# Kernel optimization log

Hardware: AMD Instinct MI355X
Metric: run time of the kernel (lower is better)

Reference implementation:

```python
import jax, jax.numpy as jnp
import numpy as np

N_NODES = 50000
N_EDGES = 800000
IN_DIM, HID_DIM, OUT_DIM = 256, 128, 64


def gcn_conv(x, edge_index, W, b):
    """PyG GCNConv: out = D^{-1/2} (A + I) D^{-1/2} (x @ W) + b."""
    n = x.shape[0]
    loops = jnp.arange(n, dtype=edge_index.dtype)
    src = jnp.concatenate([edge_index[0], loops])  # message source j
    dst = jnp.concatenate([edge_index[1], loops])  # aggregation target i
    ones = jnp.ones(src.shape[0], dtype=x.dtype)
    deg = jax.ops.segment_sum(ones, dst, num_segments=n)  # >= 1 (self-loops)
    dinv = jax.lax.rsqrt(deg)
    norm = dinv[src] * dinv[dst]                    # [E+N]
    h = x @ W                                       # [N, out] GEMM first (PyG order)
    msg = h[src] * norm[:, None]                    # gather + scale
    out = jax.ops.segment_sum(msg, dst, num_segments=n)  # scatter-add
    return out + b


def setup_inputs() -> dict:
    key = jax.random.key(0)
    k1, k2, k3, k4, k5 = jax.random.split(key, 5)
    x = jax.random.normal(k1, (N_NODES, IN_DIM), dtype=jnp.float32)
    edge_index = jax.random.randint(k2, (2, N_EDGES), 0, N_NODES, dtype=jnp.int64)
    # Glorot-ish init for weights, zero bias (PyG defaults)
    W1 = jax.random.normal(k3, (IN_DIM, HID_DIM), dtype=jnp.float32) / np.sqrt(IN_DIM)
    b1 = jnp.zeros((HID_DIM,), dtype=jnp.float32)
    W2 = jax.random.normal(k4, (HID_DIM, OUT_DIM), dtype=jnp.float32) / np.sqrt(HID_DIM)
    b2 = jnp.zeros((OUT_DIM,), dtype=jnp.float32)
    return {"x": x, "edge_index": edge_index, "W1": W1, "b1": b1, "W2": W2, "b2": b2}


def reference(x, edge_index, W1, b1, W2, b2):
    h = jax.nn.relu(gcn_conv(x, edge_index, W1, b1))
    return gcn_conv(h, edge_index, W2, b2)
```

## Files before the change

kernel.cpp:

```cpp
#include <hip/hip_runtime.h>

#define N_NODES 50000
#define N_EDGES 800000
#define IN_DIM 256
#define HID_DIM 128
#define OUT_DIM 64
#define CAP 64

typedef __bf16 bf16x8 __attribute__((ext_vector_type(8)));
typedef float f32x4 __attribute__((ext_vector_type(4)));
typedef unsigned short u16x8 __attribute__((ext_vector_type(8)));
typedef unsigned short ushort_t;
typedef unsigned int uint_t;

__device__ __forceinline__ ushort_t f2bf(float f) {
    uint_t u = __float_as_uint(f);
    return (ushort_t)((u + 0x7fffu + ((u >> 16) & 1u)) >> 16);
}
__device__ __forceinline__ float bf_lo(uint_t u) { return __uint_as_float(u << 16); }
__device__ __forceinline__ float bf_hi(uint_t u) { return __uint_as_float(u & 0xffff0000u); }

__global__ __launch_bounds__(256) void k_init(const float* __restrict__ W1,
                                              ushort_t* __restrict__ w1t,
                                              const float* __restrict__ W2,
                                              ushort_t* __restrict__ w2t) {
    const int bid = blockIdx.x;
    const int t = threadIdx.x;
    if (bid < 128) {
        int id = bid * 256 + t;
        int k = id >> 7, c = id & 127;
        w1t[c * IN_DIM + k] = f2bf(W1[id]);
    } else {
        int id = (bid - 128) * 256 + t;
        int k = id >> 6, c = id & 63;
        w2t[c * HID_DIM + k] = f2bf(W2[id]);
    }
}

__global__ __launch_bounds__(256) void k_bucket(const int* __restrict__ srcs,
                                                const int* __restrict__ dsts,
                                                int* __restrict__ cur,
                                                int* __restrict__ es) {
    int e = blockIdx.x * 256 + threadIdx.x;
    int d = dsts[e];
    int s = srcs[e];
    int p = atomicAdd(&cur[d << 4], 1);
    if (p < CAP) es[d * CAP + p] = s;
}

__global__ __launch_bounds__(256) void k_dinv(const int* __restrict__ cur,
                                              float* __restrict__ dinv,
                                              int* __restrict__ ndeg) {
    int i = blockIdx.x * 256 + threadIdx.x;
    if (i < N_NODES) {
        int deg = cur[i << 4];
        dinv[i] = rsqrtf((float)(deg + 1));
        ndeg[i] = min(deg, CAP);
    }
}

__global__ __launch_bounds__(64) void k_gemm1(const float* __restrict__ x,
                                              const ushort_t* __restrict__ w1t,
                                              ushort_t* __restrict__ hb) {
    const int lane = threadIdx.x;
    const int l15 = lane & 15, quad = lane >> 4;
    const int row = blockIdx.x * 16 + l15;
    f32x4 acc[8];
#pragma unroll
    for (int n = 0; n < 8; ++n) acc[n] = (f32x4){0.f, 0.f, 0.f, 0.f};
    const float* xrow = x + (size_t)row * IN_DIM + quad * 8;
    const ushort_t* wbase = w1t + quad * 8;
#pragma unroll
    for (int t = 0; t < 8; ++t) {
        const float4* xp = (const float4*)(xrow + t * 32);
        float4 f0 = xp[0], f1 = xp[1];
        u16x8 au;
        au[0] = f2bf(f0.x); au[1] = f2bf(f0.y); au[2] = f2bf(f0.z); au[3] = f2bf(f0.w);
        au[4] = f2bf(f1.x); au[5] = f2bf(f1.y); au[6] = f2bf(f1.z); au[7] = f2bf(f1.w);
        bf16x8 a = __builtin_bit_cast(bf16x8, au);
#pragma unroll
        for (int n = 0; n < 8; ++n) {
            bf16x8 b = *(const bf16x8*)(wbase + (n * 16 + l15) * IN_DIM + t * 32);
            acc[n] = __builtin_amdgcn_mfma_f32_16x16x32_bf16(a, b, acc[n], 0, 0, 0);
        }
    }
    ushort_t* hrow = hb + ((size_t)blockIdx.x * 16 + quad * 4) * HID_DIM + l15;
#pragma unroll
    for (int n = 0; n < 8; ++n)
#pragma unroll
        for (int r = 0; r < 4; ++r)
            hrow[(size_t)r * HID_DIM + n * 16] = f2bf(acc[n][r]);
}

__global__ __launch_bounds__(256) void k_agg1(const ushort_t* __restrict__ hb,
                                              const int* __restrict__ ndeg,
                                              const float* __restrict__ dinv,
                                              const int* __restrict__ es,
                                              const float* __restrict__ b,
                                              ushort_t* __restrict__ hrelu) {
    const int i = blockIdx.x * 4 + (threadIdx.x >> 6);
    const int lane = threadIdx.x & 63;
    const float dv = dinv[i];
    const int n = ndeg[i];
    int   sj = 0;
    float nmj = 0.f;
    if (lane < n) {
        sj = es[i * CAP + lane];
        nmj = dinv[sj] * dv;
    }
    uint_t u = *(const uint_t*)(hb + (size_t)i * HID_DIM + 2 * lane);
    float a0 = bf_lo(u) * dv * dv;
    float a1 = bf_hi(u) * dv * dv;
    int j = 0;
    for (; j + 4 <= n; j += 4) {
        int s0 = __shfl(sj, j),     s1 = __shfl(sj, j + 1);
        int s2 = __shfl(sj, j + 2), s3 = __shfl(sj, j + 3);
        float m0 = __shfl(nmj, j),     m1 = __shfl(nmj, j + 1);
        float m2 = __shfl(nmj, j + 2), m3 = __shfl(nmj, j + 3);
        uint_t v0 = *(const uint_t*)(hb + (size_t)s0 * HID_DIM + 2 * lane);
        uint_t v1 = *(const uint_t*)(hb + (size_t)s1 * HID_DIM + 2 * lane);
        uint_t v2 = *(const uint_t*)(hb + (size_t)s2 * HID_DIM + 2 * lane);
        uint_t v3 = *(const uint_t*)(hb + (size_t)s3 * HID_DIM + 2 * lane);
        a0 += bf_lo(v0) * m0 + bf_lo(v1) * m1 + bf_lo(v2) * m2 + bf_lo(v3) * m3;
        a1 += bf_hi(v0) * m0 + bf_hi(v1) * m1 + bf_hi(v2) * m2 + bf_hi(v3) * m3;
    }
    for (; j < n; ++j) {
        int s = __shfl(sj, j);
        float nm = __shfl(nmj, j);
        uint_t v = *(const uint_t*)(hb + (size_t)s * HID_DIM + 2 * lane);
        a0 += bf_lo(v) * nm;
        a1 += bf_hi(v) * nm;
    }
    float v0 = a0 + b[2 * lane];     v0 = v0 > 0.f ? v0 : 0.f;
    float v1 = a1 + b[2 * lane + 1]; v1 = v1 > 0.f ? v1 : 0.f;
    *(uint_t*)(hrelu + (size_t)i * HID_DIM + 2 * lane) = ((uint_t)f2bf(v1) << 16) | f2bf(v0);
}

__global__ __launch_bounds__(64) void k_gemm2(const ushort_t* __restrict__ hrelu,
                                              const ushort_t* __restrict__ w2t,
                                              ushort_t* __restrict__ h2) {
    const int lane = threadIdx.x;
    const int l15 = lane & 15, quad = lane >> 4;
    const int row = blockIdx.x * 16 + l15;
    f32x4 acc[4];
#pragma unroll
    for (int n = 0; n < 4; ++n) acc[n] = (f32x4){0.f, 0.f, 0.f, 0.f};
    const ushort_t* arow = hrelu + (size_t)row * HID_DIM + quad * 8;
    const ushort_t* wbase = w2t + quad * 8;
#pragma unroll
    for (int t = 0; t < 4; ++t) {
        bf16x8 a = *(const bf16x8*)(arow + t * 32);
#pragma unroll
        for (int n = 0; n < 4; ++n) {
            bf16x8 b = *(const bf16x8*)(wbase + (n * 16 + l15) * HID_DIM + t * 32);
            acc[n] = __builtin_amdgcn_mfma_f32_16x16x32_bf16(a, b, acc[n], 0, 0, 0);
        }
    }
    ushort_t* orow = h2 + ((size_t)blockIdx.x * 16 + quad * 4) * OUT_DIM + l15;
#pragma unroll
    for (int n = 0; n < 4; ++n)
#pragma unroll
        for (int r = 0; r < 4; ++r)
            orow[(size_t)r * OUT_DIM + n * 16] = f2bf(acc[n][r]);
}

__global__ __launch_bounds__(256) void k_agg2(const ushort_t* __restrict__ h2,
                                              const int* __restrict__ ndeg,
                                              const float* __restrict__ dinv,
                                              const int* __restrict__ es,
                                              const float* __restrict__ b,
                                              float* __restrict__ out) {
    const int i = blockIdx.x * 4 + (threadIdx.x >> 6);
    const int lane = threadIdx.x & 63;
    const float dv = dinv[i];
    const int n = ndeg[i];
    int   sj = 0;
    float nmj = 0.f;
    if (lane < n) {
        sj = es[i * CAP + lane];
        nmj = dinv[sj] * dv;
    }
    float acc = __uint_as_float(((uint_t)h2[(size_t)i * OUT_DIM + lane]) << 16) * dv * dv;
    int j = 0;
    for (; j + 4 <= n; j += 4) {
        int s0 = __shfl(sj, j),     s1 = __shfl(sj, j + 1);
        int s2 = __shfl(sj, j + 2), s3 = __shfl(sj, j + 3);
        float m0 = __shfl(nmj, j),     m1 = __shfl(nmj, j + 1);
        float m2 = __shfl(nmj, j + 2), m3 = __shfl(nmj, j + 3);
        float v0 = __uint_as_float(((uint_t)h2[(size_t)s0 * OUT_DIM + lane]) << 16);
        float v1 = __uint_as_float(((uint_t)h2[(size_t)s1 * OUT_DIM + lane]) << 16);
        float v2 = __uint_as_float(((uint_t)h2[(size_t)s2 * OUT_DIM + lane]) << 16);
        float v3 = __uint_as_float(((uint_t)h2[(size_t)s3 * OUT_DIM + lane]) << 16);
        acc += v0 * m0 + v1 * m1 + v2 * m2 + v3 * m3;
    }
    for (; j < n; ++j) {
        int s = __shfl(sj, j);
        float nm = __shfl(nmj, j);
        acc += __uint_as_float(((uint_t)h2[(size_t)s * OUT_DIM + lane]) << 16) * nm;
    }
    out[(size_t)i * OUT_DIM + lane] = acc + b[lane];
}

extern "C" void kernel_launch(void* const* d_in, const int* in_sizes, int n_in,
                              void* d_out, int out_size, void* d_ws, size_t ws_size,
                              hipStream_t stream) {
    const float* x   = (const float*)d_in[0];
    const int*   ei  = (const int*)d_in[1];
    const float* W1  = (const float*)d_in[2];
    const float* b1  = (const float*)d_in[3];
    const float* W2  = (const float*)d_in[4];
    const float* b2  = (const float*)d_in[5];
    float* out = (float*)d_out;

    const int* srcs = ei;
    const int* dsts = ei + N_EDGES;

    char* ws = (char*)d_ws;
    size_t o = 0;
    auto alloc = [&](size_t bytes) { void* p = ws + o; o = (o + bytes + 511) & ~size_t(511); return p; };
    int*      cur   = (int*)     alloc((size_t)N_NODES * 16 * 4);
    float*    dinv  = (float*)   alloc(N_NODES * 4);
    int*      ndeg  = (int*)     alloc(N_NODES * 4);
    int*      es    = (int*)     alloc((size_t)N_NODES * CAP * 4);
    ushort_t* w1t   = (ushort_t*)alloc((size_t)IN_DIM * HID_DIM * 2);
    ushort_t* w2t   = (ushort_t*)alloc((size_t)HID_DIM * OUT_DIM * 2);
    ushort_t* hb    = (ushort_t*)alloc((size_t)N_NODES * HID_DIM * 2);
    ushort_t* hrelu = (ushort_t*)alloc((size_t)N_NODES * HID_DIM * 2);
    ushort_t* h2    = (ushort_t*)alloc((size_t)N_NODES * OUT_DIM * 2);

    hipMemsetAsync(cur, 0, (size_t)N_NODES * 16 * 4, stream);
    k_init  <<<160, 256, 0, stream>>>(W1, w1t, W2, w2t);
    k_bucket<<<3125, 256, 0, stream>>>(srcs, dsts, cur, es);
    k_dinv  <<<196, 256, 0, stream>>>(cur, dinv, ndeg);
    k_gemm1 <<<N_NODES / 16, 64, 0, stream>>>(x, w1t, hb);
    k_agg1  <<<N_NODES / 4, 256, 0, stream>>>(hb, ndeg, dinv, es, b1, hrelu);
    k_gemm2 <<<N_NODES / 16, 64, 0, stream>>>(hrelu, w2t, h2);
    k_agg2  <<<N_NODES / 4, 256, 0, stream>>>(h2, ndeg, dinv, es, b2, out);
}
```

Measured before the change: 249.7 us.

## Store edge sources as uint16, fuse dinv into GEMM1, unroll gathers by eight

Edge source indices in the bucket table are stored as 16-bit values instead of 32-bit, halving the bucket write and read traffic. Each bucketing thread now handles two edges. The degree/dinv computation moves into the first GEMM kernel, removing one launch. The aggregation loops gain an 8-wide unrolled gather to keep more loads in flight. The uint16 cast truncates node ids above 65535 only if N_NODES grows; at 50000 nodes it is exact.

```diff
diff --git a/kernel.cpp b/kernel.cpp
--- a/kernel.cpp
+++ b/kernel.cpp
@@ -6,6 +6,7 @@
 #define HID_DIM 128
 #define OUT_DIM 64
 #define CAP 64
+#define HALF_E 400000
 
 typedef __bf16 bf16x8 __attribute__((ext_vector_type(8)));
 typedef float f32x4 __attribute__((ext_vector_type(4)));
@@ -40,30 +41,34 @@
 __global__ __launch_bounds__(256) void k_bucket(const int* __restrict__ srcs,
                                                 const int* __restrict__ dsts,
                                                 int* __restrict__ cur,
-                                                int* __restrict__ es) {
-    int e = blockIdx.x * 256 + threadIdx.x;
-    int d = dsts[e];
-    int s = srcs[e];
-    int p = atomicAdd(&cur[d << 4], 1);
-    if (p < CAP) es[d * CAP + p] = s;
-}
-
-__global__ __launch_bounds__(256) void k_dinv(const int* __restrict__ cur,
+                                                ushort_t* __restrict__ es) {
+    int t = blockIdx.x * 256 + threadIdx.x;
+    if (t < HALF_E) {
+        int d0 = dsts[t];
+        int s0 = srcs[t];
+        int d1 = dsts[t + HALF_E];
+        int s1 = srcs[t + HALF_E];
+        int p0 = atomicAdd(&cur[d0 << 4], 1);
+        int p1 = atomicAdd(&cur[d1 << 4], 1);
+        if (p0 < CAP) es[d0 * CAP + p0] = (ushort_t)s0;
+        if (p1 < CAP) es[d1 * CAP + p1] = (ushort_t)s1;
+    }
+}
+
+__global__ __launch_bounds__(64) void k_gemm1(const float* __restrict__ x,
+                                              const ushort_t* __restrict__ w1t,
+                                              const int* __restrict__ cur,
                                               float* __restrict__ dinv,
-                                              int* __restrict__ ndeg) {
-    int i = blockIdx.x * 256 + threadIdx.x;
-    if (i < N_NODES) {
+                                              int* __restrict__ ndeg,
+                                              ushort_t* __restrict__ hb) {
+    const int lane = threadIdx.x;
+    const int l15 = lane & 15, quad = lane >> 4;
+    if (lane < 16) {
+        int i = blockIdx.x * 16 + lane;
         int deg = cur[i << 4];
         dinv[i] = rsqrtf((float)(deg + 1));
         ndeg[i] = min(deg, CAP);
     }
-}
-
-__global__ __launch_bounds__(64) void k_gemm1(const float* __restrict__ x,
-                                              const ushort_t* __restrict__ w1t,
-                                              ushort_t* __restrict__ hb) {
-    const int lane = threadIdx.x;
-    const int l15 = lane & 15, quad = lane >> 4;
     const int row = blockIdx.x * 16 + l15;
     f32x4 acc[8];
 #pragma unroll
@@ -95,7 +100,7 @@
 __global__ __launch_bounds__(256) void k_agg1(const ushort_t* __restrict__ hb,
                                               const int* __restrict__ ndeg,
                                               const float* __restrict__ dinv,
-                                              const int* __restrict__ es,
+                                              const ushort_t* __restrict__ es,
                                               const float* __restrict__ b,
                                               ushort_t* __restrict__ hrelu) {
     const int i = blockIdx.x * 4 + (threadIdx.x >> 6);
@@ -105,13 +110,35 @@
     int   sj = 0;
     float nmj = 0.f;
     if (lane < n) {
-        sj = es[i * CAP + lane];
+        sj = (int)es[i * CAP + lane];
         nmj = dinv[sj] * dv;
     }
     uint_t u = *(const uint_t*)(hb + (size_t)i * HID_DIM + 2 * lane);
     float a0 = bf_lo(u) * dv * dv;
     float a1 = bf_hi(u) * dv * dv;
     int j = 0;
+    for (; j + 8 <= n; j += 8) {
+        int s0 = __shfl(sj, j),     s1 = __shfl(sj, j + 1);
+        int s2 = __shfl(sj, j + 2), s3 = __shfl(sj, j + 3);
+        int s4 = __shfl(sj, j + 4), s5 = __shfl(sj, j + 5);
+        int s6 = __shfl(sj, j + 6), s7 = __shfl(sj, j + 7);
+        float m0 = __shfl(nmj, j),     m1 = __shfl(nmj, j + 1);
+        float m2 = __shfl(nmj, j + 2), m3 = __shfl(nmj, j + 3);
+        float m4 = __shfl(nmj, j + 4), m5 = __shfl(nmj, j + 5);
+        float m6 = __shfl(nmj, j + 6), m7 = __shfl(nmj, j + 7);
+        uint_t v0 = *(const uint_t*)(hb + (size_t)s0 * HID_DIM + 2 * lane);
+        uint_t v1 = *(const uint_t*)(hb + (size_t)s1 * HID_DIM + 2 * lane);
+        uint_t v2 = *(const uint_t*)(hb + (size_t)s2 * HID_DIM + 2 * lane);
+        uint_t v3 = *(const uint_t*)(hb + (size_t)s3 * HID_DIM + 2 * lane);
+        uint_t v4 = *(const uint_t*)(hb + (size_t)s4 * HID_DIM + 2 * lane);
+        uint_t v5 = *(const uint_t*)(hb + (size_t)s5 * HID_DIM + 2 * lane);
+        uint_t v6 = *(const uint_t*)(hb + (size_t)s6 * HID_DIM + 2 * lane);
+        uint_t v7 = *(const uint_t*)(hb + (size_t)s7 * HID_DIM + 2 * lane);
+        a0 += bf_lo(v0) * m0 + bf_lo(v1) * m1 + bf_lo(v2) * m2 + bf_lo(v3) * m3
+            + bf_lo(v4) * m4 + bf_lo(v5) * m5 + bf_lo(v6) * m6 + bf_lo(v7) * m7;
+        a1 += bf_hi(v0) * m0 + bf_hi(v1) * m1 + bf_hi(v2) * m2 + bf_hi(v3) * m3
+            + bf_hi(v4) * m4 + bf_hi(v5) * m5 + bf_hi(v6) * m6 + bf_hi(v7) * m7;
+    }
     for (; j + 4 <= n; j += 4) {
         int s0 = __shfl(sj, j),     s1 = __shfl(sj, j + 1);
         int s2 = __shfl(sj, j + 2), s3 = __shfl(sj, j + 3);
@@ -167,7 +194,7 @@
 __global__ __launch_bounds__(256) void k_agg2(const ushort_t* __restrict__ h2,
                                               const int* __restrict__ ndeg,
                                               const float* __restrict__ dinv,
-                                              const int* __restrict__ es,
+                                              const ushort_t* __restrict__ es,
                                               const float* __restrict__ b,
                                               float* __restrict__ out) {
     const int i = blockIdx.x * 4 + (threadIdx.x >> 6);
@@ -177,11 +204,30 @@
     int   sj = 0;
     float nmj = 0.f;
     if (lane < n) {
-        sj = es[i * CAP + lane];
+        sj = (int)es[i * CAP + lane];
         nmj = dinv[sj] * dv;
     }
     float acc = __uint_as_float(((uint_t)h2[(size_t)i * OUT_DIM + lane]) << 16) * dv * dv;
     int j = 0;
+    for (; j + 8 <= n; j += 8) {
+        int s0 = __shfl(sj, j),     s1 = __shfl(sj, j + 1);
+        int s2 = __shfl(sj, j + 2), s3 = __shfl(sj, j + 3);
+        int s4 = __shfl(sj, j + 4), s5 = __shfl(sj, j + 5);
+        int s6 = __shfl(sj, j + 6), s7 = __shfl(sj, j + 7);
+        float m0 = __shfl(nmj, j),     m1 = __shfl(nmj, j + 1);
+        float m2 = __shfl(nmj, j + 2), m3 = __shfl(nmj, j + 3);
+        float m4 = __shfl(nmj, j + 4), m5 = __shfl(nmj, j + 5);
+        float m6 = __shfl(nmj, j + 6), m7 = __shfl(nmj, j + 7);
+        float v0 = __uint_as_float(((uint_t)h2[(size_t)s0 * OUT_DIM + lane]) << 16);
+        float v1 = __uint_as_float(((uint_t)h2[(size_t)s1 * OUT_DIM + lane]) << 16);
+        float v2 = __uint_as_float(((uint_t)h2[(size_t)s2 * OUT_DIM + lane]) << 16);
+        float v3 = __uint_as_float(((uint_t)h2[(size_t)s3 * OUT_DIM + lane]) << 16);
+        float v4 = __uint_as_float(((uint_t)h2[(size_t)s4 * OUT_DIM + lane]) << 16);
+        float v5 = __uint_as_float(((uint_t)h2[(size_t)s5 * OUT_DIM + lane]) << 16);
+        float v6 = __uint_as_float(((uint_t)h2[(size_t)s6 * OUT_DIM + lane]) << 16);
+        float v7 = __uint_as_float(((uint_t)h2[(size_t)s7 * OUT_DIM + lane]) << 16);
+        acc += v0 * m0 + v1 * m1 + v2 * m2 + v3 * m3 + v4 * m4 + v5 * m5 + v6 * m6 + v7 * m7;
+    }
     for (; j + 4 <= n; j += 4) {
         int s0 = __shfl(sj, j),     s1 = __shfl(sj, j + 1);
         int s2 = __shfl(sj, j + 2), s3 = __shfl(sj, j + 3);
@@ -221,7 +267,7 @@
     int*      cur   = (int*)     alloc((size_t)N_NODES * 16 * 4);
     float*    dinv  = (float*)   alloc(N_NODES * 4);
     int*      ndeg  = (int*)     alloc(N_NODES * 4);
-    int*      es    = (int*)     alloc((size_t)N_NODES * CAP * 4);
+    ushort_t* es    = (ushort_t*)alloc((size_t)N_NODES * CAP * 2);
     ushort_t* w1t   = (ushort_t*)alloc((size_t)IN_DIM * HID_DIM * 2);
     ushort_t* w2t   = (ushort_t*)alloc((size_t)HID_DIM * OUT_DIM * 2);
     ushort_t* hb    = (ushort_t*)alloc((size_t)N_NODES * HID_DIM * 2);
@@ -230,9 +276,8 @@
 
     hipMemsetAsync(cur, 0, (size_t)N_NODES * 16 * 4, stream);
     k_init  <<<160, 256, 0, stream>>>(W1, w1t, W2, w2t);
-    k_bucket<<<3125, 256, 0, stream>>>(srcs, dsts, cur, es);
-    k_dinv  <<<196, 256, 0, stream>>>(cur, dinv, ndeg);
-    k_gemm1 <<<N_NODES / 16, 64, 0, stream>>>(x, w1t, hb);
+    k_bucket<<<1563, 256, 0, stream>>>(srcs, dsts, cur, es);
+    k_gemm1 <<<N_NODES / 16, 64, 0, stream>>>(x, w1t, cur, dinv, ndeg, hb);
     k_agg1  <<<N_NODES / 4, 256, 0, stream>>>(hb, ndeg, dinv, es, b1, hrelu);
     k_gemm2 <<<N_NODES / 16, 64, 0, stream>>>(hrelu, w2t, h2);
     k_agg2  <<<N_NODES / 4, 256, 0, stream>>>(h2, ndeg, dinv, es, b2, out);
```

Result: faster. 241.7 us (-3.2%).
